# Optimization experiments

Measured on AMD Instinct MI355X. Metric: run time of the kernel, lower is better.

Reference implementation:

```python
import jax, jax.numpy as jnp
import numpy as np

STRIDE = 2

def setup_inputs() -> dict:
    key = jax.random.key(0)
    k1, k2, k3, k4, k5 = jax.random.split(key, 5)
    B, Cin, H, W = 16, 64, 128, 128
    Cout, kh, kw = 64, 3, 3
    oh = ow = 63  # ceil((H - kh + 1) / STRIDE)
    inp = jax.random.normal(k1, (B, Cin, H, W), dtype=jnp.float32)
    fan_in = Cin * kh * kw
    weight = jax.random.normal(k2, (Cout, Cin, kh, kw), dtype=jnp.float32) / np.sqrt(fan_in)
    bias = jax.random.normal(k3, (Cout,), dtype=jnp.float32) * 0.01
    selh = jax.random.randint(k4, (oh, ow), 0, STRIDE, dtype=jnp.int32)
    selw = jax.random.randint(k5, (oh, ow), 0, STRIDE, dtype=jnp.int32)
    return {"input": inp, "weight": weight, "bias": bias, "selh": selh, "selw": selw}


def reference(input, weight, bias, selh, selw):
    # Stochastic downsampled conv: per output pixel (i,j), pick the patch at
    # row i*stride + selh[i,j], col j*stride + selw[i,j], then apply the conv GEMM.
    Cout, Cin, kh, kw = weight.shape
    oh, ow = selh.shape
    # top-left corner of the selected patch for each output pixel
    rng_h = selh + jnp.arange(0, oh * STRIDE, STRIDE, dtype=jnp.int32)[:, None]   # (oh, ow)
    rng_w = selw + jnp.arange(0, ow * STRIDE, STRIDE, dtype=jnp.int32)[None, :]   # (oh, ow)
    # full patch index grids: (oh, ow, kh, kw)
    ih = rng_h[:, :, None, None] + jnp.arange(kh, dtype=jnp.int32)[None, None, :, None]
    iw = rng_w[:, :, None, None] + jnp.arange(kw, dtype=jnp.int32)[None, None, None, :]
    # gather selected im2col patches only (avoids materializing the full unfold)
    patches = input[:, :, ih, iw]  # (B, Cin, oh, ow, kh, kw)
    out = jnp.einsum('bcyxhw,ochw->boyx', patches, weight) + bias[None, :, None, None]
    return out  # (B, Cout, oh, ow)
```

## Files before the change

### kernel.cpp

```cpp
#include <hip/hip_runtime.h>


#define B_    16
#define CIN   64
#define H_    128
#define W_    128
#define COUT  64
#define OH    63
#define OW    63
#define NPIX  (OH * OW)
#define KTOT  (CIN * 9)

typedef short  short8   __attribute__((ext_vector_type(8)));
typedef float  floatx16 __attribute__((ext_vector_type(16)));

__device__ inline short f2bf(float f) {
    union { float f; unsigned u; } x; x.f = f;
    unsigned r = x.u + 0x7fffu + ((x.u >> 16) & 1u);
    return (short)(r >> 16);
}

__global__ __launch_bounds__(256)
void transpose_nhwc_bf16(const float* __restrict__ in, short* __restrict__ nhwc) {
    __shared__ float T[64 * 65];
    const int tid = threadIdx.x;
    const int w0  = blockIdx.x * 64;
    const int h   = blockIdx.y;
    const int b   = blockIdx.z;

    {
        const int w4 = tid & 15;
        const int cl = tid >> 4;
#pragma unroll
        for (int i = 0; i < 4; ++i) {
            const int c = cl + 16 * i;
            const float4 v = *(const float4*)&in[((b * CIN + c) * H_ + h) * W_ + w0 + 4 * w4];
            T[c * 65 + 4 * w4 + 0] = v.x;
            T[c * 65 + 4 * w4 + 1] = v.y;
            T[c * 65 + 4 * w4 + 2] = v.z;
            T[c * 65 + 4 * w4 + 3] = v.w;
        }
    }
    __syncthreads();
    {
        const int cg = tid & 7;
        const int wl = tid >> 3;
#pragma unroll
        for (int i = 0; i < 2; ++i) {
            const int w = wl + 32 * i;
            short8 v;
#pragma unroll
            for (int t = 0; t < 8; ++t)
                v[t] = f2bf(T[(8 * cg + t) * 65 + w]);
            *(short8*)&nhwc[((b * H_ + h) * W_ + w0 + w) * CIN + 8 * cg] = v;
        }
    }
}

__global__ __launch_bounds__(576)
void transpose_wgt_bf16(const float* __restrict__ wgt, short* __restrict__ wgt_t) {
    const int o = blockIdx.x;
    const int t = threadIdx.x;
    const int c = t / 9;
    const int tap = t - c * 9;
    wgt_t[o * KTOT + tap * CIN + c] = f2bf(wgt[o * KTOT + c * 9 + tap]);
}

#define PIXT  16
#define BT    4
#define LDO   68

__global__ __launch_bounds__(256, 2)
void sconv2davg_mfma(const short* __restrict__ nhwc,
                     const short* __restrict__ wgt_t,
                     const float* __restrict__ bias,
                     const int* __restrict__ selh,
                     const int* __restrict__ selw,
                     float* __restrict__ out) {
    __shared__ __align__(16) short WL[72 * 64 * 8];

    const int tid = threadIdx.x;
    const int p0  = blockIdx.x * PIXT;
    const int b0  = blockIdx.y * BT;

    const int lane = tid & 63;
    const int wv   = tid >> 6;
    const int ln32 = lane & 31;
    const int h    = lane >> 5;
    const int mw   = wv & 1;
    const int nw   = wv >> 1;
    const int m0   = mw * 32;
    const int o0   = nw * 32;

#pragma unroll
    for (int i = 0; i < 18; ++i) {
        const int idx = i * 256 + tid;
        const int o   = idx & 63;
        const int g   = idx >> 6;
        *(short8*)&WL[(g * 64 + o) * 8] = *(const short8*)&wgt_t[o * KTOT + g * 8];
    }

    const int m  = m0 + ln32;
    const int pl = m >> 2;
    const int bl = m & 3;
    int p = p0 + pl;
    if (p > NPIX - 1) p = NPIX - 1;
    const int y = p / OW;
    const int x = p - y * OW;
    const int ih0 = 2 * y + selh[p];
    const int iw0 = 2 * x + selw[p];
    const short* __restrict__ arow =
        nhwc + (((size_t)(b0 + bl) * H_ + ih0) * W_ + iw0) * CIN;

    __syncthreads();

    short8 areg[36];
#pragma unroll
    for (int tap = 0; tap < 9; ++tap) {
        const int kh = tap / 3, kw = tap - 3 * (tap / 3);
#pragma unroll
        for (int q = 0; q < 4; ++q)
            areg[tap * 4 + q] = *(const short8*)&arow[(kh * W_ + kw) * CIN + q * 16 + h * 8];
    }

    floatx16 acc0 = {0.f}, acc1 = {0.f};
#pragma unroll
    for (int s = 0; s < 36; s += 2) {
        const short8 b0f = *(const short8*)&WL[(((s + 0) * 2 + h) * 64 + o0 + ln32) * 8];
        acc0 = __builtin_amdgcn_mfma_f32_32x32x16_bf16(areg[s + 0], b0f, acc0, 0, 0, 0);
        const short8 b1f = *(const short8*)&WL[(((s + 1) * 2 + h) * 64 + o0 + ln32) * 8];
        acc1 = __builtin_amdgcn_mfma_f32_32x32x16_bf16(areg[s + 1], b1f, acc1, 0, 0, 0);
    }

    __syncthreads();

    float* Ot = (float*)WL;
    const float bv = bias[o0 + ln32];
#pragma unroll
    for (int r = 0; r < 16; ++r) {
        const int row = (r & 3) + 8 * (r >> 2) + 4 * h;
        Ot[(m0 + row) * LDO + o0 + ln32] = acc0[r] + acc1[r] + bv;
    }
    __syncthreads();
    {
        const int o  = tid & 63;
        const int b2 = tid >> 6;
        const int rowbase = ((b0 + b2) * COUT + o) * NPIX;
#pragma unroll
        for (int pp = 0; pp < PIXT; ++pp) {
            const int pw = p0 + pp;
            if (pw < NPIX)
                out[rowbase + pw] = Ot[(pp * 4 + b2) * LDO + o];
        }
    }
}

#define FKC   72
#define FLDA  76
__global__ __launch_bounds__(256, 4)
void sconv2davg_fallback(const float* __restrict__ in,
                         const float* __restrict__ wgt,
                         const float* __restrict__ bias,
                         const int* __restrict__ selh,
                         const int* __restrict__ selw,
                         float* __restrict__ out) {
    __shared__ float As[64 * FLDA];
    __shared__ float Ws[64 * FLDA];
    __shared__ int hb_s[4], wb_s[4];
    const int tid = threadIdx.x;
    const int p0  = blockIdx.x * 4;
    if (tid < 4) {
        int p = p0 + tid;
        if (p > NPIX - 1) p = NPIX - 1;
        int y = p / OW;
        int x = p - y * OW;
        hb_s[tid] = 2 * y + selh[p];
        wb_s[tid] = 2 * x + selw[p];
    }
    __syncthreads();
    const int tn = tid & 15, tm = tid >> 4;
    float acc[4][4];
#pragma unroll
    for (int i = 0; i < 4; ++i)
#pragma unroll
        for (int j = 0; j < 4; ++j) acc[i][j] = 0.0f;
    for (int cc = 0; cc < 8; ++cc) {
        const int c0 = cc * 8;
#pragma unroll
        for (int it = 0; it < 18; ++it) {
            int idx = tid + it * 256;
            int m = idx / FKC, rem = idx - m * FKC;
            int cl = rem / 9, r = rem - cl * 9;
            int kh = r / 3, kw = r - kh * 3;
            As[m * FLDA + rem] =
                in[((((m & 15) * CIN) + (c0 + cl)) * H_ + hb_s[m >> 4] + kh) * W_ + wb_s[m >> 4] + kw];
        }
#pragma unroll
        for (int it = 0; it < 18; ++it) {
            int idx = tid + it * 256;
            int o = idx / FKC, kk = idx - o * FKC;
            Ws[o * FLDA + kk] = wgt[o * KTOT + cc * FKC + kk];
        }
        __syncthreads();
#pragma unroll 2
        for (int k0 = 0; k0 < FKC; k0 += 4) {
            float4 a[4], w[4];
#pragma unroll
            for (int i = 0; i < 4; ++i) a[i] = *(const float4*)&As[(4 * tm + i) * FLDA + k0];
#pragma unroll
            for (int j = 0; j < 4; ++j) w[j] = *(const float4*)&Ws[(tn + 16 * j) * FLDA + k0];
#pragma unroll
            for (int i = 0; i < 4; ++i)
#pragma unroll
                for (int j = 0; j < 4; ++j) {
                    acc[i][j] += a[i].x * w[j].x; acc[i][j] += a[i].y * w[j].y;
                    acc[i][j] += a[i].z * w[j].z; acc[i][j] += a[i].w * w[j].w;
                }
        }
        __syncthreads();
    }
    const int p = p0 + (tm >> 2);
    if (p < NPIX) {
#pragma unroll
        for (int i = 0; i < 4; ++i) {
            int b = (tm & 3) * 4 + i;
#pragma unroll
            for (int j = 0; j < 4; ++j)
                out[((b * COUT) + tn + 16 * j) * NPIX + p] = acc[i][j] + bias[tn + 16 * j];
        }
    }
}

extern "C" void kernel_launch(void* const* d_in, const int* in_sizes, int n_in,
                              void* d_out, int out_size, void* d_ws, size_t ws_size,
                              hipStream_t stream) {
    const float* in   = (const float*)d_in[0];
    const float* wgt  = (const float*)d_in[1];
    const float* bias = (const float*)d_in[2];
    const int*   selh = (const int*)d_in[3];
    const int*   selw = (const int*)d_in[4];
    float* out = (float*)d_out;

    const size_t nhwc_elems = (size_t)B_ * H_ * W_ * CIN;
    const size_t need = (nhwc_elems + (size_t)COUT * KTOT) * 2;

    if (ws_size >= need) {
        short* nhwc  = (short*)d_ws;
        short* wgt_t = nhwc + nhwc_elems;
        transpose_nhwc_bf16<<<dim3(W_ / 64, H_, B_), 256, 0, stream>>>(in, nhwc);
        transpose_wgt_bf16<<<COUT, 576, 0, stream>>>(wgt, wgt_t);
        const int ptiles = (NPIX + PIXT - 1) / PIXT;
        sconv2davg_mfma<<<dim3(ptiles, B_ / BT), 256, 0, stream>>>(
            nhwc, wgt_t, bias, selh, selw, out);
    } else {
        sconv2davg_fallback<<<(NPIX + 3) / 4, 256, 0, stream>>>(
            in, wgt, bias, selh, selw, out);
    }
}
```

Before: 150.1 us.

## Stage A and weight tiles in LDS per channel chunk for higher occupancy

The MFMA conv kernel no longer preloads the whole 36-fragment A row into registers and the full weight matrix into LDS. It now loops over four 16-channel chunks. In each chunk, half the block gathers the selected input patches into LDS and the other half loads the matching weight slice, then 9 MFMAs consume them. This cuts LDS use and register pressure so the kernel can run 4 blocks per CU. The cost is extra barriers per chunk, no overlap between loading and compute within a block, and a single serially dependent accumulator. The output row mapping is reordered to batch-major to match the new A layout.

```diff
diff --git a/kernel.cpp b/kernel.cpp
--- a/kernel.cpp
+++ b/kernel.cpp
@@ -68,78 +68,95 @@
 
 #define PIXT  16
 #define BT    4
+#define LDK   144
 #define LDO   68
 
-__global__ __launch_bounds__(256, 2)
+__global__ __launch_bounds__(256, 4)
 void sconv2davg_mfma(const short* __restrict__ nhwc,
                      const short* __restrict__ wgt_t,
                      const float* __restrict__ bias,
                      const int* __restrict__ selh,
                      const int* __restrict__ selw,
                      float* __restrict__ out) {
-    __shared__ __align__(16) short WL[72 * 64 * 8];
+    __shared__ __align__(16) short As[64 * LDK];
+    __shared__ __align__(16) short Ws[64 * LDK];
+    __shared__ int ab_s[PIXT];
 
     const int tid = threadIdx.x;
     const int p0  = blockIdx.x * PIXT;
     const int b0  = blockIdx.y * BT;
 
+    if (tid < PIXT) {
+        int p = p0 + tid;
+        if (p > NPIX - 1) p = NPIX - 1;
+        int y = p / OW;
+        int x = p - y * OW;
+        ab_s[tid] = (2 * y + selh[p]) * W_ + (2 * x + selw[p]);
+    }
+    __syncthreads();
+
     const int lane = tid & 63;
     const int wv   = tid >> 6;
     const int ln32 = lane & 31;
-    const int h    = lane >> 5;
+    const int h2   = lane >> 5;
     const int mw   = wv & 1;
     const int nw   = wv >> 1;
-    const int m0   = mw * 32;
-    const int o0   = nw * 32;
-
-#pragma unroll
-    for (int i = 0; i < 18; ++i) {
-        const int idx = i * 256 + tid;
-        const int o   = idx & 63;
-        const int g   = idx >> 6;
-        *(short8*)&WL[(g * 64 + o) * 8] = *(const short8*)&wgt_t[o * KTOT + g * 8];
-    }
-
-    const int m  = m0 + ln32;
-    const int pl = m >> 2;
-    const int bl = m & 3;
-    int p = p0 + pl;
-    if (p > NPIX - 1) p = NPIX - 1;
-    const int y = p / OW;
-    const int x = p - y * OW;
-    const int ih0 = 2 * y + selh[p];
-    const int iw0 = 2 * x + selw[p];
-    const short* __restrict__ arow =
-        nhwc + (((size_t)(b0 + bl) * H_ + ih0) * W_ + iw0) * CIN;
-
-    __syncthreads();
-
-    short8 areg[36];
-#pragma unroll
-    for (int tap = 0; tap < 9; ++tap) {
-        const int kh = tap / 3, kw = tap - 3 * (tap / 3);
-#pragma unroll
-        for (int q = 0; q < 4; ++q)
-            areg[tap * 4 + q] = *(const short8*)&arow[(kh * W_ + kw) * CIN + q * 16 + h * 8];
-    }
-
-    floatx16 acc0 = {0.f}, acc1 = {0.f};
-#pragma unroll
-    for (int s = 0; s < 36; s += 2) {
-        const short8 b0f = *(const short8*)&WL[(((s + 0) * 2 + h) * 64 + o0 + ln32) * 8];
-        acc0 = __builtin_amdgcn_mfma_f32_32x32x16_bf16(areg[s + 0], b0f, acc0, 0, 0, 0);
-        const short8 b1f = *(const short8*)&WL[(((s + 1) * 2 + h) * 64 + o0 + ln32) * 8];
-        acc1 = __builtin_amdgcn_mfma_f32_32x32x16_bf16(areg[s + 1], b1f, acc1, 0, 0, 0);
-    }
-
-    __syncthreads();
-
-    float* Ot = (float*)WL;
-    const float bv = bias[o0 + ln32];
+
+    const int stid = tid & 127;
+
+    floatx16 acc = {0.f};
+
+#pragma unroll
+    for (int cc = 0; cc < 4; ++cc) {
+        const int c0 = cc * 16;
+        if (cc) __syncthreads();
+
+        if (tid < 128) {
+#pragma unroll
+            for (int i = 0; i < 9; ++i) {
+                const int u    = i * 128 + stid;
+                const int mm   = u / 18;
+                const int r    = u - mm * 18;
+                const int tap  = r >> 1;
+                const int half = r & 1;
+                const int kh   = tap / 3;
+                const int kw   = tap - 3 * kh;
+                const int bl_  = mm >> 4;
+                const int pl_  = mm & 15;
+                const short* src = nhwc
+                    + ((size_t)(b0 + bl_) * H_ * W_ + ab_s[pl_] + kh * W_ + kw) * CIN
+                    + c0 + half * 8;
+                *(short8*)&As[mm * LDK + tap * 16 + half * 8] = *(const short8*)src;
+            }
+        } else {
+#pragma unroll
+            for (int i = 0; i < 9; ++i) {
+                const int u    = i * 128 + stid;
+                const int o    = u / 18;
+                const int r    = u - o * 18;
+                const int tap  = r >> 1;
+                const int half = r & 1;
+                *(short8*)&Ws[o * LDK + tap * 16 + half * 8] =
+                    *(const short8*)&wgt_t[o * KTOT + tap * CIN + c0 + half * 8];
+            }
+        }
+        __syncthreads();
+
+#pragma unroll
+        for (int tap = 0; tap < 9; ++tap) {
+            const short8 a = *(const short8*)&As[(mw * 32 + ln32) * LDK + tap * 16 + h2 * 8];
+            const short8 b = *(const short8*)&Ws[(nw * 32 + ln32) * LDK + tap * 16 + h2 * 8];
+            acc = __builtin_amdgcn_mfma_f32_32x32x16_bf16(a, b, acc, 0, 0, 0);
+        }
+    }
+
+    __syncthreads();
+    float* Ot = (float*)As;
+    const float bv = bias[nw * 32 + ln32];
 #pragma unroll
     for (int r = 0; r < 16; ++r) {
-        const int row = (r & 3) + 8 * (r >> 2) + 4 * h;
-        Ot[(m0 + row) * LDO + o0 + ln32] = acc0[r] + acc1[r] + bv;
+        const int row = (r & 3) + 8 * (r >> 2) + 4 * h2;
+        Ot[(mw * 32 + row) * LDO + nw * 32 + ln32] = acc[r] + bv;
     }
     __syncthreads();
     {
@@ -150,7 +167,7 @@
         for (int pp = 0; pp < PIXT; ++pp) {
             const int pw = p0 + pp;
             if (pw < NPIX)
-                out[rowbase + pw] = Ot[(pp * 4 + b2) * LDO + o];
+                out[rowbase + pw] = Ot[(b2 * 16 + pp) * LDO + o];
         }
     }
 }
```

Result: no change. 151.5 us (+1.0%).

## Pre-swizzle weights in LDS layout and load them via direct global-to-LDS DMA

Applied to the files above, without the earlier changes.

The weight transpose kernel now writes weights in the exact LDS tile layout, so the conv kernel fills shared memory with global_load_lds DMA instead of a register round-trip. The A-operand gathers are issued before a single waitcnt/barrier so that the weight DMA and activation loads overlap. The row mapping also changes to pixel-major within each batch (m = bl*16 + pl), which makes the epilogue store loop read contiguous pixel rows. This depends on the global_load_lds builtin semantics and on the wave-uniform LDS base being correct.

```diff
diff --git a/kernel.cpp b/kernel.cpp
--- a/kernel.cpp
+++ b/kernel.cpp
@@ -14,6 +14,13 @@
 typedef short  short8   __attribute__((ext_vector_type(8)));
 typedef float  floatx16 __attribute__((ext_vector_type(16)));
 
+#define AS1 __attribute__((address_space(1)))
+#define AS3 __attribute__((address_space(3)))
+
+__device__ __forceinline__ void dma16(const short* g, short* l) {
+    __builtin_amdgcn_global_load_lds((const AS1 void*)g, (AS3 void*)l, 16, 0, 0);
+}
+
 __device__ inline short f2bf(float f) {
     union { float f; unsigned u; } x; x.f = f;
     unsigned r = x.u + 0x7fffu + ((x.u >> 16) & 1u);
@@ -58,12 +65,13 @@
 }
 
 __global__ __launch_bounds__(576)
-void transpose_wgt_bf16(const float* __restrict__ wgt, short* __restrict__ wgt_t) {
+void transpose_wgt_bf16(const float* __restrict__ wgt, short* __restrict__ wgt2) {
     const int o = blockIdx.x;
     const int t = threadIdx.x;
     const int c = t / 9;
     const int tap = t - c * 9;
-    wgt_t[o * KTOT + tap * CIN + c] = f2bf(wgt[o * KTOT + c * 9 + tap]);
+    const int g = tap * 8 + (c >> 3);
+    wgt2[(g * 64 + o) * 8 + (c & 7)] = f2bf(wgt[o * KTOT + c * 9 + tap]);
 }
 
 #define PIXT  16
@@ -72,37 +80,32 @@
 
 __global__ __launch_bounds__(256, 2)
 void sconv2davg_mfma(const short* __restrict__ nhwc,
-                     const short* __restrict__ wgt_t,
+                     const short* __restrict__ wgt2,
                      const float* __restrict__ bias,
                      const int* __restrict__ selh,
                      const int* __restrict__ selw,
                      float* __restrict__ out) {
     __shared__ __align__(16) short WL[72 * 64 * 8];
 
-    const int tid = threadIdx.x;
-    const int p0  = blockIdx.x * PIXT;
-    const int b0  = blockIdx.y * BT;
-
+    const int tid  = threadIdx.x;
     const int lane = tid & 63;
     const int wv   = tid >> 6;
     const int ln32 = lane & 31;
-    const int h    = lane >> 5;
+    const int h2   = lane >> 5;
     const int mw   = wv & 1;
     const int nw   = wv >> 1;
-    const int m0   = mw * 32;
-    const int o0   = nw * 32;
+    const int p0   = blockIdx.x * PIXT;
+    const int b0   = blockIdx.y * BT;
 
 #pragma unroll
     for (int i = 0; i < 18; ++i) {
-        const int idx = i * 256 + tid;
-        const int o   = idx & 63;
-        const int g   = idx >> 6;
-        *(short8*)&WL[(g * 64 + o) * 8] = *(const short8*)&wgt_t[o * KTOT + g * 8];
-    }
-
-    const int m  = m0 + ln32;
-    const int pl = m >> 2;
-    const int bl = m & 3;
+        const int ub = i * 256 + wv * 64;
+        dma16(wgt2 + ((size_t)ub + lane) * 8, &WL[ub * 8]);
+    }
+
+    const int m  = mw * 32 + ln32;
+    const int bl = m >> 4;
+    const int pl = m & 15;
     int p = p0 + pl;
     if (p > NPIX - 1) p = NPIX - 1;
     const int y = p / OW;
@@ -110,36 +113,38 @@
     const int ih0 = 2 * y + selh[p];
     const int iw0 = 2 * x + selw[p];
     const short* __restrict__ arow =
-        nhwc + (((size_t)(b0 + bl) * H_ + ih0) * W_ + iw0) * CIN;
-
-    __syncthreads();
+        nhwc + (((size_t)(b0 + bl) * H_ + ih0) * W_ + iw0) * CIN + h2 * 8;
 
     short8 areg[36];
 #pragma unroll
-    for (int tap = 0; tap < 9; ++tap) {
+    for (int s = 0; s < 36; ++s) {
+        const int tap = s >> 2, q = s & 3;
         const int kh = tap / 3, kw = tap - 3 * (tap / 3);
-#pragma unroll
-        for (int q = 0; q < 4; ++q)
-            areg[tap * 4 + q] = *(const short8*)&arow[(kh * W_ + kw) * CIN + q * 16 + h * 8];
-    }
+        areg[s] = *(const short8*)&arow[(kh * W_ + kw) * CIN + q * 16];
+    }
+    __builtin_amdgcn_sched_barrier(0);
+    asm volatile("s_waitcnt vmcnt(0)" ::: "memory");
+    __syncthreads();
 
     floatx16 acc0 = {0.f}, acc1 = {0.f};
 #pragma unroll
     for (int s = 0; s < 36; s += 2) {
-        const short8 b0f = *(const short8*)&WL[(((s + 0) * 2 + h) * 64 + o0 + ln32) * 8];
+        const short8 b0f = *(const short8*)
+            &WL[(((s + 0) * 2 + h2) * 64 + nw * 32 + ln32) * 8];
         acc0 = __builtin_amdgcn_mfma_f32_32x32x16_bf16(areg[s + 0], b0f, acc0, 0, 0, 0);
-        const short8 b1f = *(const short8*)&WL[(((s + 1) * 2 + h) * 64 + o0 + ln32) * 8];
+        const short8 b1f = *(const short8*)
+            &WL[(((s + 1) * 2 + h2) * 64 + nw * 32 + ln32) * 8];
         acc1 = __builtin_amdgcn_mfma_f32_32x32x16_bf16(areg[s + 1], b1f, acc1, 0, 0, 0);
     }
 
     __syncthreads();
 
     float* Ot = (float*)WL;
-    const float bv = bias[o0 + ln32];
+    const float bv = bias[nw * 32 + ln32];
 #pragma unroll
     for (int r = 0; r < 16; ++r) {
-        const int row = (r & 3) + 8 * (r >> 2) + 4 * h;
-        Ot[(m0 + row) * LDO + o0 + ln32] = acc0[r] + acc1[r] + bv;
+        const int row = (r & 3) + 8 * (r >> 2) + 4 * h2;
+        Ot[(mw * 32 + row) * LDO + nw * 32 + ln32] = acc0[r] + acc1[r] + bv;
     }
     __syncthreads();
     {
@@ -150,7 +155,7 @@
         for (int pp = 0; pp < PIXT; ++pp) {
             const int pw = p0 + pp;
             if (pw < NPIX)
-                out[rowbase + pw] = Ot[(pp * 4 + b2) * LDO + o];
+                out[rowbase + pw] = Ot[(b2 * 16 + pp) * LDO + o];
         }
     }
 }
@@ -245,13 +250,13 @@
     const size_t need = (nhwc_elems + (size_t)COUT * KTOT) * 2;
 
     if (ws_size >= need) {
-        short* nhwc  = (short*)d_ws;
-        short* wgt_t = nhwc + nhwc_elems;
+        short* nhwc = (short*)d_ws;
+        short* wgt2 = nhwc + nhwc_elems;
         transpose_nhwc_bf16<<<dim3(W_ / 64, H_, B_), 256, 0, stream>>>(in, nhwc);
-        transpose_wgt_bf16<<<COUT, 576, 0, stream>>>(wgt, wgt_t);
+        transpose_wgt_bf16<<<COUT, 576, 0, stream>>>(wgt, wgt2);
         const int ptiles = (NPIX + PIXT - 1) / PIXT;
         sconv2davg_mfma<<<dim3(ptiles, B_ / BT), 256, 0, stream>>>(
-            nhwc, wgt_t, bias, selh, selw, out);
+            nhwc, wgt2, bias, selh, selw, out);
     } else {
         sconv2davg_fallback<<<(NPIX + 3) / 4, 256, 0, stream>>>(
             in, wgt, bias, selh, selw, out);
```

After: 146.9 us. 1.02x faster.
